# Optimization experiments

Hardware: AMD Instinct MI355X
Metric: run time of the kernel (lower is better)

## Reference

```python
import jax, jax.numpy as jnp
import numpy as np

B, L, DATA, W, H, VFH, LAB = 4, 128, 6, 5, 64, 128, 10
NUM_STEPS = 2248
LOGSIG_LEN = (L - 1) // 8 + 1           # 16, since idx = searchsorted(ts, t)//8
LS_DIM = 1 + W + W * (W - 1) // 2        # 16: const + letters + depth-2 brackets


def _linear_init(key, out_dim, in_dim):
    lim = 1.0 / np.sqrt(in_dim)
    kw, kb = jax.random.split(key)
    w = jax.random.uniform(kw, (out_dim, in_dim), minval=-lim, maxval=lim, dtype=jnp.float32)
    b = jax.random.uniform(kb, (out_dim,), minval=-lim, maxval=lim, dtype=jnp.float32)
    return w, b


def setup_inputs() -> dict:
    key = jax.random.key(0)
    ks = jax.random.split(key, 8)
    l1_w, l1_b = _linear_init(ks[0], H, W)           # linear1: width -> hidden
    l2_w, l2_b = _linear_init(ks[1], LAB, H)         # linear2: hidden -> labels
    vf_w0, vf_b0 = _linear_init(ks[2], VFH, H)       # vf MLP: H -> VFH -> VFH -> W*H
    vf_w1, vf_b1 = _linear_init(ks[3], VFH, VFH)
    vf_w2, vf_b2 = _linear_init(ks[4], W * H, VFH)
    # Hall-set depth-2 pairs (1-indexed letters), matching hs.data[1:][W:]
    pairs = jnp.asarray(np.array([(a, b) for a in range(1, W + 1) for b in range(a + 1, W + 1)], dtype=np.int32))
    return {
        "ts": jnp.linspace(0.0, 1.0, L, dtype=jnp.float32),
        "logsig": jax.random.normal(ks[5], (B, LOGSIG_LEN, LS_DIM), dtype=jnp.float32) * 0.05,
        "x0": jax.random.normal(ks[6], (B, DATA), dtype=jnp.float32),
        "l1_w": l1_w, "l1_b": l1_b, "l2_w": l2_w, "l2_b": l2_b,
        "vf_w0": vf_w0, "vf_b0": vf_b0, "vf_w1": vf_w1, "vf_b1": vf_b1,
        "vf_w2": vf_w2, "vf_b2": vf_b2,
        "pairs": pairs,
        "num_steps": NUM_STEPS,
    }


def reference(ts, logsig, x0, l1_w, l1_b, l2_w, l2_b,
              vf_w0, vf_b0, vf_w1, vf_b1, vf_w2, vf_b2, pairs, num_steps):
    def vf(y):  # neural vector field: H -> W*H, tanh MLP
        h = jnp.tanh(vf_w0 @ y + vf_b0)
        h = jnp.tanh(vf_w1 @ h + vf_b1)
        return jnp.tanh(vf_w2 @ h + vf_b2)

    ia = pairs[:, 0] - 1
    ib = pairs[:, 1] - 1

    def field(t, y, ls_seq):
        idx = jnp.minimum(jnp.searchsorted(ts, t) // 8, ls_seq.shape[0] - 1)
        ls = ls_seq[idx]
        vf_out = vf(y).reshape(W, H)                                  # [W, H]
        # Jacobian-vector products along each vector-field column
        jvps = jax.vmap(lambda tx: jax.jvp(vf, (y,), (tx,))[1])(vf_out).reshape(W, W, H)
        lie = jvps[ib, ia] - jvps[ia, ib]                             # [P, H] Lie brackets
        return ls[1:W + 1] @ vf_out + ls[W + 1:] @ lie                # [H]

    t0 = ts[0]
    dt = (ts[-1] - ts[0]) / num_steps

    def integrate(y0, ls_seq):  # fixed-step Heun
        def step(y, i):
            t = t0 + i.astype(y.dtype) * dt
            k1 = field(t, y, ls_seq)
            k2 = field(t + dt, y + dt * k1, ls_seq)
            return y + 0.5 * dt * (k1 + k2), None
        yT, _ = jax.lax.scan(step, y0, jnp.arange(num_steps))
        return yT

    y0 = x0[:, 1:] @ l1_w.T + l1_b                                    # drop time channel
    yT = jax.vmap(integrate)(y0, logsig)                              # [B, H]
    return jax.nn.softmax(yT @ l2_w.T + l2_b, axis=-1)                # [B, LAB]
```

## Files before the change

### kernel.cpp

```cpp
#include <hip/hip_runtime.h>
#include <math.h>

#define BLOCK   512
#define HD      64
#define VFH     128
#define WD      5
#define NPAIR   10
#define LSDIM   16
#define LSLEN   16
#define TSN     128
#define OUTD    (WD*HD)

__device__ __forceinline__ float dpp_xor1(float x) {
    return __int_as_float(__builtin_amdgcn_mov_dpp(__float_as_int(x), 0xB1, 0xF, 0xF, false));
}
__device__ __forceinline__ float dpp_xor2(float x) {
    return __int_as_float(__builtin_amdgcn_mov_dpp(__float_as_int(x), 0x4E, 0xF, 0xF, false));
}
__device__ __forceinline__ float dot4(float4 a, float4 b) {
    return a.x*b.x + a.y*b.y + a.z*b.z + a.w*b.w;
}

__global__ __launch_bounds__(BLOCK, 2)
void lncde_kernel(const float* __restrict__ ts, const float* __restrict__ logsig,
                  const float* __restrict__ x0,
                  const float* __restrict__ l1w, const float* __restrict__ l1b,
                  const float* __restrict__ l2w, const float* __restrict__ l2b,
                  const float* __restrict__ w0g, const float* __restrict__ b0g,
                  const float* __restrict__ w1g, const float* __restrict__ b1g,
                  const float* __restrict__ w2g, const float* __restrict__ b2g,
                  const int* __restrict__ pairs, const int* __restrict__ nsp,
                  float* __restrict__ outp, int dataDim)
{
    __shared__ float sTs[TSN];
    __shared__ float sLs[LSLEN * LSDIM];
    __shared__ float sH0[VFH], sH1[VFH];
    __shared__ float sOut[OUTD];
    __shared__ float sT[WD * HD];
    __shared__ float sDh[WD * VFH];
    __shared__ float sU[WD * VFH];
    __shared__ float sPart[OUTD];
    __shared__ float sY[HD], sY2[HD], sK1[HD];

    const int tid  = threadIdx.x;
    const int b    = blockIdx.x;
    const int row  = tid >> 2;
    const int part = tid & 3;
    const int gw   = tid >> 6;

    for (int i = tid; i < TSN; i += BLOCK)           sTs[i] = ts[i];
    for (int i = tid; i < LSLEN * LSDIM; i += BLOCK) sLs[i] = logsig[b * LSLEN * LSDIM + i];

    float4 w0r[4];
    #pragma unroll
    for (int k = 0; k < 4; ++k) w0r[k] = *(const float4*)(w0g + tid * 16 + 4 * k);
    float4 w1r[8];
    #pragma unroll
    for (int k = 0; k < 8; ++k) w1r[k] = *(const float4*)(w1g + tid * 32 + 4 * k);
    const float b0r = b0g[row];
    const float b1r = b1g[row];

    float4 w2r[32];
    float b2r = 0.f;
    if (tid < OUTD) {
        #pragma unroll
        for (int k = 0; k < 32; ++k) w2r[k] = *(const float4*)(w2g + tid * VFH + 4 * k);
        b2r = b2g[tid];
    } else {
        #pragma unroll
        for (int k = 0; k < 32; ++k) w2r[k] = make_float4(0.f, 0.f, 0.f, 0.f);
    }

    const int  q0 = 0 + (0 >= gw), q1 = 1 + (1 >= gw), q2 = 2 + (2 >= gw), q3 = 3 + (3 >= gw);
    #define PAIR_IDX(lo, hi) ((lo) * (9 - (lo)) / 2 + ((hi) - (lo) - 1))
    const int  p0 = (q0 > gw) ? PAIR_IDX(gw, q0) : PAIR_IDX(q0, gw);
    const int  p1 = (q1 > gw) ? PAIR_IDX(gw, q1) : PAIR_IDX(q1, gw);
    const int  p2 = (q2 > gw) ? PAIR_IDX(gw, q2) : PAIR_IDX(q2, gw);
    const int  p3 = (q3 > gw) ? PAIR_IDX(gw, q3) : PAIR_IDX(q3, gw);
    const float g0 = (q0 > gw) ? 1.f : -1.f;
    const float g1 = (q1 > gw) ? 1.f : -1.f;
    const float g2 = (q2 > gw) ? 1.f : -1.f;
    const float g3 = (q3 > gw) ? 1.f : -1.f;

    __syncthreads();

    if (tid < HD) {
        float acc = l1b[tid];
        #pragma unroll
        for (int w = 0; w < WD; ++w) acc += x0[b * dataDim + 1 + w] * l1w[tid * WD + w];
        sY[tid] = acc;
    }
    const float t0v    = sTs[0];
    const int   nsteps = nsp[0];
    const float dtv    = (sTs[TSN - 1] - t0v) / (float)nsteps;
    __syncthreads();

    auto field = [&](float t, const float* __restrict__ yv, int mode) {
        int cnt = 0;
        #pragma unroll
        for (int s = 64; s > 0; s >>= 1) {
            int c2 = cnt + s;
            if (c2 <= TSN && sTs[c2 - 1] < t) cnt = c2;
        }
        int il = cnt >> 3; il = il > (LSLEN - 1) ? (LSLEN - 1) : il;
        const float* ls = &sLs[il * LSDIM];

        float d0v;
        {
            float acc = 0.f;
            #pragma unroll
            for (int k = 0; k < 4; ++k) {
                float4 y4 = *(const float4*)&yv[part * 16 + 4 * k];
                acc += dot4(w0r[k], y4);
            }
            acc += dpp_xor1(acc); acc += dpp_xor2(acc);
            float h = tanhf(acc + b0r); d0v = 1.f - h * h;
            if (part == 0) sH0[row] = h;
        }
        __syncthreads();
        float d1v;
        {
            float acc = 0.f;
            #pragma unroll
            for (int k = 0; k < 8; ++k) {
                float4 x4 = *(const float4*)&sH0[part * 32 + 4 * k];
                acc += dot4(w1r[k], x4);
            }
            acc += dpp_xor1(acc); acc += dpp_xor2(acc);
            float h = tanhf(acc + b1r); d1v = 1.f - h * h;
            if (part == 0) sH1[row] = h;
        }
        __syncthreads();
        float outv = 0.f, derv = 0.f;
        if (tid < OUTD) {
            float acc = 0.f;
            #pragma unroll
            for (int k = 0; k < 32; ++k) {
                float4 x4 = *(const float4*)&sH1[4 * k];
                acc += dot4(w2r[k], x4);
            }
            outv = tanhf(acc + b2r); derv = 1.f - outv * outv;
            sOut[tid] = outv;
        }
        __syncthreads();
        if (tid < OUTD) {
            int th = tid & 63;
            float tv = g0 * ls[6 + p0] * sOut[q0 * HD + th]
                     + g1 * ls[6 + p1] * sOut[q1 * HD + th]
                     + g2 * ls[6 + p2] * sOut[q2 * HD + th]
                     + g3 * ls[6 + p3] * sOut[q3 * HD + th];
            sT[gw * HD + th] = tv;
        }
        __syncthreads();
        #pragma unroll
        for (int w = 0; w < WD; ++w) {
            float acc = 0.f;
            #pragma unroll
            for (int k = 0; k < 4; ++k) {
                float4 x4 = *(const float4*)&sT[w * HD + part * 16 + 4 * k];
                acc += dot4(w0r[k], x4);
            }
            acc += dpp_xor1(acc); acc += dpp_xor2(acc);
            if (part == 0) sDh[w * VFH + row] = d0v * acc;
        }
        __syncthreads();
        #pragma unroll
        for (int w = 0; w < WD; ++w) {
            float acc = 0.f;
            #pragma unroll
            for (int k = 0; k < 8; ++k) {
                float4 x4 = *(const float4*)&sDh[w * VFH + part * 32 + 4 * k];
                acc += dot4(w1r[k], x4);
            }
            acc += dpp_xor1(acc); acc += dpp_xor2(acc);
            if (part == 0) sU[w * VFH + row] = d1v * acc;
        }
        __syncthreads();
        if (tid < OUTD) {
            const float* up = &sU[gw * VFH];
            float acc = 0.f;
            #pragma unroll
            for (int k = 0; k < 32; ++k) {
                float4 x4 = *(const float4*)&up[4 * k];
                acc += dot4(w2r[k], x4);
            }
            sPart[tid] = ls[1 + gw] * outv + derv * acc;
        }
        __syncthreads();
        if (tid < HD) {
            float kv = sPart[tid] + sPart[HD + tid] + sPart[2 * HD + tid]
                     + sPart[3 * HD + tid] + sPart[4 * HD + tid];
            if (mode == 0) { sK1[tid] = kv; sY2[tid] = sY[tid] + dtv * kv; }
            else           { sY[tid] = sY[tid] + 0.5f * dtv * (sK1[tid] + kv); }
        }
        __syncthreads();
    };

    for (int i = 0; i < nsteps; ++i) {
        float t = t0v + (float)i * dtv;
        field(t, sY, 0);
        field(t + dtv, sY2, 1);
    }

    if (tid == 0) {
        float lg[10];
        float mx = -3.4e38f;
        #pragma unroll
        for (int l = 0; l < 10; ++l) {
            float acc = l2b[l];
            for (int h = 0; h < HD; ++h) acc += sY[h] * l2w[l * HD + h];
            lg[l] = acc; mx = fmaxf(mx, acc);
        }
        float sum = 0.f;
        #pragma unroll
        for (int l = 0; l < 10; ++l) { lg[l] = expf(lg[l] - mx); sum += lg[l]; }
        float inv = 1.f / sum;
        #pragma unroll
        for (int l = 0; l < 10; ++l) outp[b * 10 + l] = lg[l] * inv;
    }
}

extern "C" void kernel_launch(void* const* d_in, const int* in_sizes, int n_in,
                              void* d_out, int out_size, void* d_ws, size_t ws_size,
                              hipStream_t stream) {
    const float* ts     = (const float*)d_in[0];
    const float* logsig = (const float*)d_in[1];
    const float* x0     = (const float*)d_in[2];
    const float* l1w    = (const float*)d_in[3];
    const float* l1b    = (const float*)d_in[4];
    const float* l2w    = (const float*)d_in[5];
    const float* l2b    = (const float*)d_in[6];
    const float* w0     = (const float*)d_in[7];
    const float* b0     = (const float*)d_in[8];
    const float* w1     = (const float*)d_in[9];
    const float* b1     = (const float*)d_in[10];
    const float* w2     = (const float*)d_in[11];
    const float* b2     = (const float*)d_in[12];
    const int*   pairs  = (const int*)d_in[13];
    const int*   nsp    = (const int*)d_in[14];
    float* outp = (float*)d_out;

    const int B = in_sizes[1] / (LSLEN * LSDIM);
    const int dataDim = in_sizes[2] / (B > 0 ? B : 1);

    hipLaunchKernelGGL(lncde_kernel, dim3(B), dim3(BLOCK), 0, stream,
                       ts, logsig, x0, l1w, l1b, l2w, l2b,
                       w0, b0, w1, b1, w2, b2, pairs, nsp, outp, dataDim);
}
```

Before: 20.21 ms.

## Use packed FMA dot products, pad LDS buffers, and pin weight registers

Replaces the scalar float4 dot products with v_pk_fma_f32 packed FMAs using two interleaved accumulators. The sH0 and sDh shared buffers are padded to reduce LDS bank conflicts on the per-quarter strided reads. The W2 weights move into 32 named register variables loaded for every thread, with upper threads aliasing valid rows so the dense-layer dot product needs no branch. Empty asm statements pin all weight registers live across the time loop so the compiler does not spill or rematerialise them. The cost is higher register pressure and dot-product work in threads whose results are discarded.

```diff
diff --git a/kernel.cpp b/kernel.cpp
--- a/kernel.cpp
+++ b/kernel.cpp
@@ -10,6 +10,11 @@
 #define LSLEN   16
 #define TSN     128
 #define OUTD    (WD*HD)
+#define PCH     36
+#define PADIDX(i) ((((i) >> 5) * PCH) + ((i) & 31))
+
+using f32x4 = __attribute__((ext_vector_type(4))) float;
+using f32x2 = __attribute__((ext_vector_type(2))) float;
 
 __device__ __forceinline__ float dpp_xor1(float x) {
     return __int_as_float(__builtin_amdgcn_mov_dpp(__float_as_int(x), 0xB1, 0xF, 0xF, false));
@@ -17,9 +22,20 @@
 __device__ __forceinline__ float dpp_xor2(float x) {
     return __int_as_float(__builtin_amdgcn_mov_dpp(__float_as_int(x), 0x4E, 0xF, 0xF, false));
 }
-__device__ __forceinline__ float dot4(float4 a, float4 b) {
-    return a.x*b.x + a.y*b.y + a.z*b.z + a.w*b.w;
-}
+__device__ __forceinline__ void pkfma(f32x2& acc, f32x2 a, f32x2 b) {
+    asm("v_pk_fma_f32 %0, %1, %2, %0" : "+v"(acc) : "v"(a), "v"(b));
+}
+__device__ __forceinline__ void dot4pk(f32x2& acc, f32x4 w, f32x4 x) {
+    f32x2 wl = {w[0], w[1]}, wh = {w[2], w[3]};
+    f32x2 xl = {x[0], x[1]}, xh = {x[2], x[3]};
+    pkfma(acc, wl, xl);
+    pkfma(acc, wh, xh);
+}
+
+#define W2_LIST(OP) OP(0) OP(1) OP(2) OP(3) OP(4) OP(5) OP(6) OP(7) \
+    OP(8) OP(9) OP(10) OP(11) OP(12) OP(13) OP(14) OP(15) \
+    OP(16) OP(17) OP(18) OP(19) OP(20) OP(21) OP(22) OP(23) \
+    OP(24) OP(25) OP(26) OP(27) OP(28) OP(29) OP(30) OP(31)
 
 __global__ __launch_bounds__(BLOCK, 2)
 void lncde_kernel(const float* __restrict__ ts, const float* __restrict__ logsig,
@@ -34,10 +50,11 @@
 {
     __shared__ float sTs[TSN];
     __shared__ float sLs[LSLEN * LSDIM];
-    __shared__ float sH0[VFH], sH1[VFH];
+    __shared__ float sH0p[4 * PCH];
+    __shared__ float sH1[VFH];
     __shared__ float sOut[OUTD];
     __shared__ float sT[WD * HD];
-    __shared__ float sDh[WD * VFH];
+    __shared__ float sDhp[WD * 4 * PCH];
     __shared__ float sU[WD * VFH];
     __shared__ float sPart[OUTD];
     __shared__ float sY[HD], sY2[HD], sK1[HD];
@@ -47,29 +64,23 @@
     const int row  = tid >> 2;
     const int part = tid & 3;
     const int gw   = tid >> 6;
+    const int rowc = (tid < OUTD) ? tid : (tid - 192);
 
     for (int i = tid; i < TSN; i += BLOCK)           sTs[i] = ts[i];
     for (int i = tid; i < LSLEN * LSDIM; i += BLOCK) sLs[i] = logsig[b * LSLEN * LSDIM + i];
 
-    float4 w0r[4];
+    f32x4 w0r[4];
     #pragma unroll
-    for (int k = 0; k < 4; ++k) w0r[k] = *(const float4*)(w0g + tid * 16 + 4 * k);
-    float4 w1r[8];
+    for (int k = 0; k < 4; ++k) w0r[k] = *(const f32x4*)(w0g + tid * 16 + 4 * k);
+    f32x4 w1r[8];
     #pragma unroll
-    for (int k = 0; k < 8; ++k) w1r[k] = *(const float4*)(w1g + tid * 32 + 4 * k);
+    for (int k = 0; k < 8; ++k) w1r[k] = *(const f32x4*)(w1g + tid * 32 + 4 * k);
     const float b0r = b0g[row];
     const float b1r = b1g[row];
-
-    float4 w2r[32];
-    float b2r = 0.f;
-    if (tid < OUTD) {
-        #pragma unroll
-        for (int k = 0; k < 32; ++k) w2r[k] = *(const float4*)(w2g + tid * VFH + 4 * k);
-        b2r = b2g[tid];
-    } else {
-        #pragma unroll
-        for (int k = 0; k < 32; ++k) w2r[k] = make_float4(0.f, 0.f, 0.f, 0.f);
-    }
+    const float b2r = b2g[rowc];
+
+#define W2_DECL(n) f32x4 w2_##n = *(const f32x4*)(w2g + rowc * VFH + 4 * (n));
+    W2_LIST(W2_DECL)
 
     const int  q0 = 0 + (0 >= gw), q1 = 1 + (1 >= gw), q2 = 2 + (2 >= gw), q3 = 3 + (3 >= gw);
     #define PAIR_IDX(lo, hi) ((lo) * (9 - (lo)) / 2 + ((hi) - (lo) - 1))
@@ -107,40 +118,38 @@
 
         float d0v;
         {
-            float acc = 0.f;
-            #pragma unroll
-            for (int k = 0; k < 4; ++k) {
-                float4 y4 = *(const float4*)&yv[part * 16 + 4 * k];
-                acc += dot4(w0r[k], y4);
-            }
+            f32x2 a2 = {0.f, 0.f};
+            #pragma unroll
+            for (int k = 0; k < 4; ++k)
+                dot4pk(a2, w0r[k], *(const f32x4*)&yv[part * 16 + 4 * k]);
+            float acc = a2[0] + a2[1];
             acc += dpp_xor1(acc); acc += dpp_xor2(acc);
             float h = tanhf(acc + b0r); d0v = 1.f - h * h;
-            if (part == 0) sH0[row] = h;
+            if (part == 0) sH0p[PADIDX(row)] = h;
         }
         __syncthreads();
         float d1v;
         {
-            float acc = 0.f;
-            #pragma unroll
-            for (int k = 0; k < 8; ++k) {
-                float4 x4 = *(const float4*)&sH0[part * 32 + 4 * k];
-                acc += dot4(w1r[k], x4);
-            }
+            f32x2 a2 = {0.f, 0.f}, b2a = {0.f, 0.f};
+            #pragma unroll
+            for (int k = 0; k < 8; ++k)
+                dot4pk((k & 1) ? b2a : a2, w1r[k], *(const f32x4*)&sH0p[part * PCH + 4 * k]);
+            float acc = a2[0] + a2[1] + b2a[0] + b2a[1];
             acc += dpp_xor1(acc); acc += dpp_xor2(acc);
             float h = tanhf(acc + b1r); d1v = 1.f - h * h;
             if (part == 0) sH1[row] = h;
         }
         __syncthreads();
         float outv = 0.f, derv = 0.f;
-        if (tid < OUTD) {
-            float acc = 0.f;
-            #pragma unroll
-            for (int k = 0; k < 32; ++k) {
-                float4 x4 = *(const float4*)&sH1[4 * k];
-                acc += dot4(w2r[k], x4);
+        {
+            f32x2 accD0 = {0.f, 0.f}, accD1 = {0.f, 0.f};
+#define W2_DOTD(n) dot4pk(((n) & 1) ? accD1 : accD0, w2_##n, *(const f32x4*)&sH1[4 * (n)]);
+            W2_LIST(W2_DOTD)
+            if (tid < OUTD) {
+                float acc = accD0[0] + accD0[1] + accD1[0] + accD1[1];
+                outv = tanhf(acc + b2r); derv = 1.f - outv * outv;
+                sOut[tid] = outv;
             }
-            outv = tanhf(acc + b2r); derv = 1.f - outv * outv;
-            sOut[tid] = outv;
         }
         __syncthreads();
         if (tid < OUTD) {
@@ -154,37 +163,36 @@
         __syncthreads();
         #pragma unroll
         for (int w = 0; w < WD; ++w) {
-            float acc = 0.f;
-            #pragma unroll
-            for (int k = 0; k < 4; ++k) {
-                float4 x4 = *(const float4*)&sT[w * HD + part * 16 + 4 * k];
-                acc += dot4(w0r[k], x4);
+            f32x2 a2 = {0.f, 0.f};
+            #pragma unroll
+            for (int k = 0; k < 4; ++k)
+                dot4pk(a2, w0r[k], *(const f32x4*)&sT[w * HD + part * 16 + 4 * k]);
+            float acc = a2[0] + a2[1];
+            acc += dpp_xor1(acc); acc += dpp_xor2(acc);
+            if (part == 0) sDhp[w * 4 * PCH + PADIDX(row)] = d0v * acc;
+        }
+        __syncthreads();
+        #pragma unroll
+        for (int w = 0; w < WD; ++w) {
+            f32x2 a2 = {0.f, 0.f}, b2a = {0.f, 0.f};
+            #pragma unroll
+            for (int k = 0; k < 8; ++k)
+                dot4pk((k & 1) ? b2a : a2, w1r[k],
+                       *(const f32x4*)&sDhp[w * 4 * PCH + part * PCH + 4 * k]);
+            float acc = a2[0] + a2[1] + b2a[0] + b2a[1];
+            acc += dpp_xor1(acc); acc += dpp_xor2(acc);
+            if (part == 0) sU[w * VFH + row] = d1v * acc;
+        }
+        __syncthreads();
+        {
+            const float* up = &sU[gw * VFH];
+            f32x2 accG0 = {0.f, 0.f}, accG1 = {0.f, 0.f};
+#define W2_DOTG(n) dot4pk(((n) & 1) ? accG1 : accG0, w2_##n, *(const f32x4*)&up[4 * (n)]);
+            if (tid < OUTD) {
+                W2_LIST(W2_DOTG)
+                float acc = accG0[0] + accG0[1] + accG1[0] + accG1[1];
+                sPart[tid] = ls[1 + gw] * outv + derv * acc;
             }
-            acc += dpp_xor1(acc); acc += dpp_xor2(acc);
-            if (part == 0) sDh[w * VFH + row] = d0v * acc;
-        }
-        __syncthreads();
-        #pragma unroll
-        for (int w = 0; w < WD; ++w) {
-            float acc = 0.f;
-            #pragma unroll
-            for (int k = 0; k < 8; ++k) {
-                float4 x4 = *(const float4*)&sDh[w * VFH + part * 32 + 4 * k];
-                acc += dot4(w1r[k], x4);
-            }
-            acc += dpp_xor1(acc); acc += dpp_xor2(acc);
-            if (part == 0) sU[w * VFH + row] = d1v * acc;
-        }
-        __syncthreads();
-        if (tid < OUTD) {
-            const float* up = &sU[gw * VFH];
-            float acc = 0.f;
-            #pragma unroll
-            for (int k = 0; k < 32; ++k) {
-                float4 x4 = *(const float4*)&up[4 * k];
-                acc += dot4(w2r[k], x4);
-            }
-            sPart[tid] = ls[1 + gw] * outv + derv * acc;
         }
         __syncthreads();
         if (tid < HD) {
@@ -196,7 +204,14 @@
         __syncthreads();
     };
 
+#define W2_PIN(n) asm volatile("" : "+v"(w2_##n));
     for (int i = 0; i < nsteps; ++i) {
+        W2_LIST(W2_PIN)
+        #pragma unroll
+        for (int k = 0; k < 4; ++k) asm volatile("" : "+v"(w0r[k]));
+        #pragma unroll
+        for (int k = 0; k < 8; ++k) asm volatile("" : "+v"(w1r[k]));
+
         float t = t0v + (float)i * dtv;
         field(t, sY, 0);
         field(t + dtv, sY2, 1);
```

After: 16.42 ms. 18.7% less time.

## Redistribute MLP matvecs across 640 threads with packed FMA and padded LDS

Applied to the files above, without the earlier changes.

Grows the block from 512 to 640 threads so that the W*H=320-row output layer is split 16 ways across all threads, instead of each of 320 threads holding a full 128-wide row. Each thread now owns several rows over 8-element slices, computed with v_pk_fma_f32 and reduced across lanes with DPP. Shared-memory vectors are padded (12-float stride per 8 elements) to avoid bank conflicts, and the weight registers are pinned with empty asm statements. The goal is to shorten the serial per-layer dot products and relieve register pressure, at the cost of more cross-lane reduction steps and one fewer block per CU.

```diff
diff --git a/kernel.cpp b/kernel.cpp
--- a/kernel.cpp
+++ b/kernel.cpp
@@ -1,27 +1,42 @@
 #include <hip/hip_runtime.h>
 #include <math.h>
 
-#define BLOCK   512
+#define BLOCK   640
 #define HD      64
 #define VFH     128
 #define WD      5
-#define NPAIR   10
 #define LSDIM   16
 #define LSLEN   16
 #define TSN     128
 #define OUTD    (WD*HD)
-
-__device__ __forceinline__ float dpp_xor1(float x) {
-    return __int_as_float(__builtin_amdgcn_mov_dpp(__float_as_int(x), 0xB1, 0xF, 0xF, false));
+#define PC8(i)  ((((i) >> 3) * 12) + ((i) & 7))
+#define STH     96
+#define STV     192
+
+using f32x4 = __attribute__((ext_vector_type(4))) float;
+using f32x2 = __attribute__((ext_vector_type(2))) float;
+
+#define DPPADD(x, ctrl) ((x) + __int_as_float(__builtin_amdgcn_mov_dpp(__float_as_int(x), (ctrl), 0xF, 0xF, false)))
+#define RED8(x)  do { (x) = DPPADD(x, 0xB1); (x) = DPPADD(x, 0x4E); (x) = DPPADD(x, 0x141); } while (0)
+#define RED16(x) do { (x) = DPPADD(x, 0xB1); (x) = DPPADD(x, 0x4E); (x) = DPPADD(x, 0x124); (x) = DPPADD(x, 0x128); } while (0)
+
+__device__ __forceinline__ void pkfma(f32x2& acc, f32x2 a, f32x2 b) {
+    asm("v_pk_fma_f32 %0, %1, %2, %0" : "+v"(acc) : "v"(a), "v"(b));
 }
-__device__ __forceinline__ float dpp_xor2(float x) {
-    return __int_as_float(__builtin_amdgcn_mov_dpp(__float_as_int(x), 0x4E, 0xF, 0xF, false));
+__device__ __forceinline__ float dot8pk(f32x4 wa, f32x4 wb, f32x4 xa, f32x4 xb) {
+    f32x2 acc = {0.f, 0.f};
+    f32x2 w0 = {wa[0], wa[1]}, x0 = {xa[0], xa[1]};
+    f32x2 w1 = {wa[2], wa[3]}, x1 = {xa[2], xa[3]};
+    f32x2 w2 = {wb[0], wb[1]}, x2 = {xb[0], xb[1]};
+    f32x2 w3 = {wb[2], wb[3]}, x3 = {xb[2], xb[3]};
+    pkfma(acc, w0, x0); pkfma(acc, w1, x1); pkfma(acc, w2, x2); pkfma(acc, w3, x3);
+    return acc[0] + acc[1];
 }
-__device__ __forceinline__ float dot4(float4 a, float4 b) {
-    return a.x*b.x + a.y*b.y + a.z*b.z + a.w*b.w;
-}
-
-__global__ __launch_bounds__(BLOCK, 2)
+
+#define W2ROWS(OP) OP(0) OP(1) OP(2) OP(3) OP(4) OP(5) OP(6) OP(7)
+#define W1ROWS(OP) OP(0) OP(1) OP(2) OP(3)
+
+__global__ __launch_bounds__(BLOCK)
 void lncde_kernel(const float* __restrict__ ts, const float* __restrict__ logsig,
                   const float* __restrict__ x0,
                   const float* __restrict__ l1w, const float* __restrict__ l1b,
@@ -32,51 +47,47 @@
                   const int* __restrict__ pairs, const int* __restrict__ nsp,
                   float* __restrict__ outp, int dataDim)
 {
-    __shared__ float sTs[TSN];
-    __shared__ float sLs[LSLEN * LSDIM];
-    __shared__ float sH0[VFH], sH1[VFH];
+    __shared__ float sTs[TSN], sLs[LSLEN * LSDIM];
+    __shared__ float sB0[VFH], sB1[VFH], sB2[OUTD];
+    __shared__ float sYp[STH], sY2p[STH], sK1[HD];
+    __shared__ float sH0p[STV], sH1p[STV];
     __shared__ float sOut[OUTD];
-    __shared__ float sT[WD * HD];
-    __shared__ float sDh[WD * VFH];
-    __shared__ float sU[WD * VFH];
+    __shared__ float sTp[WD * STH];
+    __shared__ float sDhp[WD * STV], sUp[WD * STV];
     __shared__ float sPart[OUTD];
-    __shared__ float sY[HD], sY2[HD], sK1[HD];
 
     const int tid  = threadIdx.x;
     const int b    = blockIdx.x;
-    const int row  = tid >> 2;
-    const int part = tid & 3;
-    const int gw   = tid >> 6;
-
-    for (int i = tid; i < TSN; i += BLOCK)           sTs[i] = ts[i];
+    const int t512 = tid & 511;
+    const int rgE  = t512 >> 3,  partE = t512 & 7;
+    const int rgF  = t512 >> 4,  partF = t512 & 15;
+    const int rgD  = tid  >> 4,  partD = tid  & 15;
+
+    for (int i = tid; i < TSN;  i += BLOCK) sTs[i] = ts[i];
     for (int i = tid; i < LSLEN * LSDIM; i += BLOCK) sLs[i] = logsig[b * LSLEN * LSDIM + i];
-
-    float4 w0r[4];
-    #pragma unroll
-    for (int k = 0; k < 4; ++k) w0r[k] = *(const float4*)(w0g + tid * 16 + 4 * k);
-    float4 w1r[8];
-    #pragma unroll
-    for (int k = 0; k < 8; ++k) w1r[k] = *(const float4*)(w1g + tid * 32 + 4 * k);
-    const float b0r = b0g[row];
-    const float b1r = b1g[row];
-
-    float4 w2r[32];
-    float b2r = 0.f;
-    if (tid < OUTD) {
-        #pragma unroll
-        for (int k = 0; k < 32; ++k) w2r[k] = *(const float4*)(w2g + tid * VFH + 4 * k);
-        b2r = b2g[tid];
-    } else {
-        #pragma unroll
-        for (int k = 0; k < 32; ++k) w2r[k] = make_float4(0.f, 0.f, 0.f, 0.f);
-    }
-
-    const int  q0 = 0 + (0 >= gw), q1 = 1 + (1 >= gw), q2 = 2 + (2 >= gw), q3 = 3 + (3 >= gw);
-    #define PAIR_IDX(lo, hi) ((lo) * (9 - (lo)) / 2 + ((hi) - (lo) - 1))
-    const int  p0 = (q0 > gw) ? PAIR_IDX(gw, q0) : PAIR_IDX(q0, gw);
-    const int  p1 = (q1 > gw) ? PAIR_IDX(gw, q1) : PAIR_IDX(q1, gw);
-    const int  p2 = (q2 > gw) ? PAIR_IDX(gw, q2) : PAIR_IDX(q2, gw);
-    const int  p3 = (q3 > gw) ? PAIR_IDX(gw, q3) : PAIR_IDX(q3, gw);
+    for (int i = tid; i < VFH;  i += BLOCK) { sB0[i] = b0g[i]; sB1[i] = b1g[i]; }
+    for (int i = tid; i < OUTD; i += BLOCK) sB2[i] = b2g[i];
+
+    f32x4 w0a_0 = *(const f32x4*)(w0g + (2 * rgE + 0) * HD + partE * 8);
+    f32x4 w0b_0 = *(const f32x4*)(w0g + (2 * rgE + 0) * HD + partE * 8 + 4);
+    f32x4 w0a_1 = *(const f32x4*)(w0g + (2 * rgE + 1) * HD + partE * 8);
+    f32x4 w0b_1 = *(const f32x4*)(w0g + (2 * rgE + 1) * HD + partE * 8 + 4);
+#define W1_DECL(r) \
+    f32x4 w1a_##r = *(const f32x4*)(w1g + (4 * rgF + (r)) * VFH + partF * 8); \
+    f32x4 w1b_##r = *(const f32x4*)(w1g + (4 * rgF + (r)) * VFH + partF * 8 + 4);
+    W1ROWS(W1_DECL)
+#define W2_DECL(r) \
+    f32x4 w2a_##r = *(const f32x4*)(w2g + (8 * rgD + (r)) * VFH + partD * 8); \
+    f32x4 w2b_##r = *(const f32x4*)(w2g + (8 * rgD + (r)) * VFH + partD * 8 + 4);
+    W2ROWS(W2_DECL)
+
+    const int gw = tid >> 6;
+    const int q0 = 0 + (0 >= gw), q1 = 1 + (1 >= gw), q2 = 2 + (2 >= gw), q3 = 3 + (3 >= gw);
+#define PAIR_IDX(lo, hi) ((lo) * (9 - (lo)) / 2 + ((hi) - (lo) - 1))
+    const int p0 = (q0 > gw) ? PAIR_IDX(gw, q0) : PAIR_IDX(q0, gw);
+    const int p1 = (q1 > gw) ? PAIR_IDX(gw, q1) : PAIR_IDX(q1, gw);
+    const int p2 = (q2 > gw) ? PAIR_IDX(gw, q2) : PAIR_IDX(q2, gw);
+    const int p3 = (q3 > gw) ? PAIR_IDX(gw, q3) : PAIR_IDX(q3, gw);
     const float g0 = (q0 > gw) ? 1.f : -1.f;
     const float g1 = (q1 > gw) ? 1.f : -1.f;
     const float g2 = (q2 > gw) ? 1.f : -1.f;
@@ -88,7 +99,7 @@
         float acc = l1b[tid];
         #pragma unroll
         for (int w = 0; w < WD; ++w) acc += x0[b * dataDim + 1 + w] * l1w[tid * WD + w];
-        sY[tid] = acc;
+        sYp[PC8(tid)] = acc;
     }
     const float t0v    = sTs[0];
     const int   nsteps = nsp[0];
@@ -105,42 +116,59 @@
         int il = cnt >> 3; il = il > (LSLEN - 1) ? (LSLEN - 1) : il;
         const float* ls = &sLs[il * LSDIM];
 
-        float d0v;
+        float d0_0, d0_1;
+        float d1_0, d1_1, d1_2, d1_3;
+        float o0, o1, o2, o3, o4, o5, o6, o7;
+
+        if (tid < 512) {
+            f32x4 xa = *(const f32x4*)&yv[partE * 12];
+            f32x4 xb = *(const f32x4*)&yv[partE * 12 + 4];
+            float a0 = dot8pk(w0a_0, w0b_0, xa, xb);
+            float a1 = dot8pk(w0a_1, w0b_1, xa, xb);
+            RED8(a0); RED8(a1);
+            if (partE == 0) {
+                float2 bb = *(const float2*)&sB0[2 * rgE];
+                float h0 = tanhf(a0 + bb.x), h1 = tanhf(a1 + bb.y);
+                d0_0 = 1.f - h0 * h0; d0_1 = 1.f - h1 * h1;
+                *(float2*)&sH0p[PC8(2 * rgE)] = make_float2(h0, h1);
+            }
+        }
+        __syncthreads();
+        if (tid < 512) {
+            f32x4 xa = *(const f32x4*)&sH0p[partF * 12];
+            f32x4 xb = *(const f32x4*)&sH0p[partF * 12 + 4];
+            float c0 = dot8pk(w1a_0, w1b_0, xa, xb);
+            float c1 = dot8pk(w1a_1, w1b_1, xa, xb);
+            float c2 = dot8pk(w1a_2, w1b_2, xa, xb);
+            float c3 = dot8pk(w1a_3, w1b_3, xa, xb);
+            RED16(c0); RED16(c1); RED16(c2); RED16(c3);
+            if (partF == 0) {
+                f32x4 bb = *(const f32x4*)&sB1[4 * rgF];
+                float h0 = tanhf(c0 + bb[0]), h1 = tanhf(c1 + bb[1]);
+                float h2 = tanhf(c2 + bb[2]), h3 = tanhf(c3 + bb[3]);
+                d1_0 = 1.f - h0 * h0; d1_1 = 1.f - h1 * h1;
+                d1_2 = 1.f - h2 * h2; d1_3 = 1.f - h3 * h3;
+                f32x4 hv = {h0, h1, h2, h3};
+                *(f32x4*)&sH1p[PC8(4 * rgF)] = hv;
+            }
+        }
+        __syncthreads();
         {
-            float acc = 0.f;
-            #pragma unroll
-            for (int k = 0; k < 4; ++k) {
-                float4 y4 = *(const float4*)&yv[part * 16 + 4 * k];
-                acc += dot4(w0r[k], y4);
-            }
-            acc += dpp_xor1(acc); acc += dpp_xor2(acc);
-            float h = tanhf(acc + b0r); d0v = 1.f - h * h;
-            if (part == 0) sH0[row] = h;
-        }
-        __syncthreads();
-        float d1v;
-        {
-            float acc = 0.f;
-            #pragma unroll
-            for (int k = 0; k < 8; ++k) {
-                float4 x4 = *(const float4*)&sH0[part * 32 + 4 * k];
-                acc += dot4(w1r[k], x4);
-            }
-            acc += dpp_xor1(acc); acc += dpp_xor2(acc);
-            float h = tanhf(acc + b1r); d1v = 1.f - h * h;
-            if (part == 0) sH1[row] = h;
-        }
-        __syncthreads();
-        float outv = 0.f, derv = 0.f;
-        if (tid < OUTD) {
-            float acc = 0.f;
-            #pragma unroll
-            for (int k = 0; k < 32; ++k) {
-                float4 x4 = *(const float4*)&sH1[4 * k];
-                acc += dot4(w2r[k], x4);
-            }
-            outv = tanhf(acc + b2r); derv = 1.f - outv * outv;
-            sOut[tid] = outv;
+            f32x4 xa = *(const f32x4*)&sH1p[partD * 12];
+            f32x4 xb = *(const f32x4*)&sH1p[partD * 12 + 4];
+#define W2_DOTD(r) float aD##r = dot8pk(w2a_##r, w2b_##r, xa, xb); RED16(aD##r);
+            W2ROWS(W2_DOTD)
+            if (partD == 0) {
+                f32x4 ba = *(const f32x4*)&sB2[8 * rgD];
+                f32x4 bc = *(const f32x4*)&sB2[8 * rgD + 4];
+                o0 = tanhf(aD0 + ba[0]); o1 = tanhf(aD1 + ba[1]);
+                o2 = tanhf(aD2 + ba[2]); o3 = tanhf(aD3 + ba[3]);
+                o4 = tanhf(aD4 + bc[0]); o5 = tanhf(aD5 + bc[1]);
+                o6 = tanhf(aD6 + bc[2]); o7 = tanhf(aD7 + bc[3]);
+                f32x4 va = {o0, o1, o2, o3}, vb = {o4, o5, o6, o7};
+                *(f32x4*)&sOut[8 * rgD]     = va;
+                *(f32x4*)&sOut[8 * rgD + 4] = vb;
+            }
         }
         __syncthreads();
         if (tid < OUTD) {
@@ -149,57 +177,80 @@
                      + g1 * ls[6 + p1] * sOut[q1 * HD + th]
                      + g2 * ls[6 + p2] * sOut[q2 * HD + th]
                      + g3 * ls[6 + p3] * sOut[q3 * HD + th];
-            sT[gw * HD + th] = tv;
-        }
-        __syncthreads();
-        #pragma unroll
-        for (int w = 0; w < WD; ++w) {
-            float acc = 0.f;
+            sTp[gw * STH + PC8(th)] = tv;
+        }
+        __syncthreads();
+        if (tid < 512) {
             #pragma unroll
-            for (int k = 0; k < 4; ++k) {
-                float4 x4 = *(const float4*)&sT[w * HD + part * 16 + 4 * k];
-                acc += dot4(w0r[k], x4);
-            }
-            acc += dpp_xor1(acc); acc += dpp_xor2(acc);
-            if (part == 0) sDh[w * VFH + row] = d0v * acc;
-        }
-        __syncthreads();
-        #pragma unroll
-        for (int w = 0; w < WD; ++w) {
-            float acc = 0.f;
+            for (int w = 0; w < WD; ++w) {
+                f32x4 xa = *(const f32x4*)&sTp[w * STH + partE * 12];
+                f32x4 xb = *(const f32x4*)&sTp[w * STH + partE * 12 + 4];
+                float a0 = dot8pk(w0a_0, w0b_0, xa, xb);
+                float a1 = dot8pk(w0a_1, w0b_1, xa, xb);
+                RED8(a0); RED8(a1);
+                if (partE == 0)
+                    *(float2*)&sDhp[w * STV + PC8(2 * rgE)] = make_float2(d0_0 * a0, d0_1 * a1);
+            }
+        }
+        __syncthreads();
+        if (tid < 512) {
             #pragma unroll
-            for (int k = 0; k < 8; ++k) {
-                float4 x4 = *(const float4*)&sDh[w * VFH + part * 32 + 4 * k];
-                acc += dot4(w1r[k], x4);
-            }
-            acc += dpp_xor1(acc); acc += dpp_xor2(acc);
-            if (part == 0) sU[w * VFH + row] = d1v * acc;
-        }
-        __syncthreads();
-        if (tid < OUTD) {
-            const float* up = &sU[gw * VFH];
-            float acc = 0.f;
-            #pragma unroll
-            for (int k = 0; k < 32; ++k) {
-                float4 x4 = *(const float4*)&up[4 * k];
-                acc += dot4(w2r[k], x4);
-            }
-            sPart[tid] = ls[1 + gw] * outv + derv * acc;
+            for (int w = 0; w < WD; ++w) {
+                f32x4 xa = *(const f32x4*)&sDhp[w * STV + partF * 12];
+                f32x4 xb = *(const f32x4*)&sDhp[w * STV + partF * 12 + 4];
+                float c0 = dot8pk(w1a_0, w1b_0, xa, xb);
+                float c1 = dot8pk(w1a_1, w1b_1, xa, xb);
+                float c2 = dot8pk(w1a_2, w1b_2, xa, xb);
+                float c3 = dot8pk(w1a_3, w1b_3, xa, xb);
+                RED16(c0); RED16(c1); RED16(c2); RED16(c3);
+                if (partF == 0) {
+                    f32x4 uv = {d1_0 * c0, d1_1 * c1, d1_2 * c2, d1_3 * c3};
+                    *(f32x4*)&sUp[w * STV + PC8(4 * rgF)] = uv;
+                }
+            }
+        }
+        __syncthreads();
+        {
+            const int wb = rgD >> 3;
+            f32x4 xa = *(const f32x4*)&sUp[wb * STV + partD * 12];
+            f32x4 xb = *(const f32x4*)&sUp[wb * STV + partD * 12 + 4];
+#define W2_DOTG(r) float aG##r = dot8pk(w2a_##r, w2b_##r, xa, xb); RED16(aG##r);
+            W2ROWS(W2_DOTG)
+            if (partD == 0) {
+                float lsw = ls[1 + wb];
+                f32x4 pa = {lsw * o0 + (1.f - o0 * o0) * aG0,
+                            lsw * o1 + (1.f - o1 * o1) * aG1,
+                            lsw * o2 + (1.f - o2 * o2) * aG2,
+                            lsw * o3 + (1.f - o3 * o3) * aG3};
+                f32x4 pb = {lsw * o4 + (1.f - o4 * o4) * aG4,
+                            lsw * o5 + (1.f - o5 * o5) * aG5,
+                            lsw * o6 + (1.f - o6 * o6) * aG6,
+                            lsw * o7 + (1.f - o7 * o7) * aG7};
+                *(f32x4*)&sPart[8 * rgD]     = pa;
+                *(f32x4*)&sPart[8 * rgD + 4] = pb;
+            }
         }
         __syncthreads();
         if (tid < HD) {
             float kv = sPart[tid] + sPart[HD + tid] + sPart[2 * HD + tid]
                      + sPart[3 * HD + tid] + sPart[4 * HD + tid];
-            if (mode == 0) { sK1[tid] = kv; sY2[tid] = sY[tid] + dtv * kv; }
-            else           { sY[tid] = sY[tid] + 0.5f * dtv * (sK1[tid] + kv); }
+            float yy = sYp[PC8(tid)];
+            if (mode == 0) { sK1[tid] = kv; sY2p[PC8(tid)] = yy + dtv * kv; }
+            else           { sYp[PC8(tid)] = yy + 0.5f * dtv * (sK1[tid] + kv); }
         }
         __syncthreads();
     };
 
+#define W2_PIN(r) asm volatile("" : "+v"(w2a_##r), "+v"(w2b_##r));
+#define W1_PIN(r) asm volatile("" : "+v"(w1a_##r), "+v"(w1b_##r));
     for (int i = 0; i < nsteps; ++i) {
+        W2ROWS(W2_PIN)
+        W1ROWS(W1_PIN)
+        asm volatile("" : "+v"(w0a_0), "+v"(w0b_0), "+v"(w0a_1), "+v"(w0b_1));
+
         float t = t0v + (float)i * dtv;
-        field(t, sY, 0);
-        field(t + dtv, sY2, 1);
+        field(t, sYp, 0);
+        field(t + dtv, sY2p, 1);
     }
 
     if (tid == 0) {
@@ -208,7 +259,7 @@
         #pragma unroll
         for (int l = 0; l < 10; ++l) {
             float acc = l2b[l];
-            for (int h = 0; h < HD; ++h) acc += sY[h] * l2w[l * HD + h];
+            for (int h = 0; h < HD; ++h) acc += sYp[PC8(h)] * l2w[l * HD + h];
             lg[l] = acc; mx = fmaxf(mx, acc);
         }
         float sum = 0.f;
```

New measurement: 27.15 ms. 1.34x slower.
